# Kernel tuning notes

Hardware: AMD Instinct MI355X
Metric: run time of the kernel (lower is better)

The kernel has to match this reference:

```python
import jax, jax.numpy as jnp
import numpy as np

K = 2
ALPHA = 1.0
EPS = 1e-6


def _bce_logits(x, z):
    # binary_cross_entropy_with_logits, elementwise, numerically stable
    return jax.nn.softplus(x) - x * z


def _unfold(x, i):
    # F.unfold(x, kernel_size=2i+1, padding=i) for x: [B,1,H,W] -> [B, P, H*W]
    ks = 2 * i + 1
    p = jax.lax.conv_general_dilated_patches(
        x, (ks, ks), (1, 1), [(i, i), (i, i)])  # [B, ks*ks, H, W], zero-padded
    B = x.shape[0]
    return p.reshape(B, ks * ks, -1)


def setup_inputs() -> dict:
    key = jax.random.key(0)
    k1, k2 = jax.random.split(key)
    B, H, W = 8, 512, 512
    pred = jax.random.normal(k1, (B, 1, H, W), dtype=jnp.float32)
    target = jax.random.randint(k2, (B, 1, H, W), 0, 2).astype(jnp.float32)
    return {"pred": pred, "target": target}


def reference(pred, target):
    B, _, H, W = pred.shape
    N = H * W
    bce = _bce_logits(pred, target).reshape(B, 1, N)  # [B,1,N]
    total = jnp.zeros((B, N), dtype=pred.dtype)
    for i in range(1, K + 1):
        ks = 2 * i + 1
        P = ks * ks
        c = P // 2
        up = _unfold(pred, i)                      # [B,P,N]
        ut = _unfold(target, i)                    # [B,P,N]
        vm = _unfold(jnp.ones_like(target), i) == 0  # True where padding
        cp = up[:, c:c + 1, :]                     # center logits [B,1,N]
        ct = ut[:, c:c + 1, :]
        joint = cp * up
        lab = ct * ut
        mutual = _bce_logits(joint, lab)
        pairwise = jnp.exp(-jax.nn.sigmoid(cp) * jax.nn.sigmoid(up))
        loss = bce / (mutual + ALPHA * pairwise + EPS)
        loss = jnp.where(vm, jnp.asarray(1.0, loss.dtype), loss)
        total = total + (0.5 ** (i - 1)) * (loss.sum(axis=1) / P)
    return total.mean()
```

## Files before the change

### kernel.cpp

```cpp
#include <hip/hip_runtime.h>

#define TILE 16
#define HALO 2
#define LH (TILE + HALO)
#define LW (TILE + 2 * HALO)
#define HT 512
#define WD 512

typedef _Float16 h2 __attribute__((ext_vector_type(2)));

constexpr float W_IN  = 1.0f / 9.0f + 0.02f;
constexpr float W_OUT = 0.02f;
constexpr float INV_D_OOB = 0.590364f;


__device__ __forceinline__ h2 pk2(float a, float b) {
    return __builtin_bit_cast(h2, __builtin_amdgcn_cvt_pkrtz(a, b));
}
__device__ __forceinline__ h2 hsp(float x) {
    h2 r; r.x = (_Float16)x; r.y = (_Float16)x; return r;
}
__device__ __forceinline__ h2 mkh(float a, float b) {
    h2 r; r.x = (_Float16)a; r.y = (_Float16)b; return r;
}

struct FracH { h2 n, d; };

__device__ __forceinline__ FracH pair2h(float cax, h2 cay, h2 caz, h2 caw,
                                        const float4 cb1, const float4 cb2, h2 wv) {
    const float j1 = cax * cb1.x, j2 = cax * cb2.x;
    const h2 J = pk2(j1, j2);
    const h2 U = pk2(__expf(-fabsf(j1)), __expf(-fabsf(j2)));
    const h2 T = pk2(cb1.y, cb2.y);
    const h2 G = pk2(cb1.z, cb2.z);
    const h2 Wb = pk2(cb1.w, cb2.w);
    h2 L = __builtin_elementwise_fma(U, hsp(0.098765f), hsp(-0.370370f));
    L = __builtin_elementwise_fma(L, U, hsp(0.962963f));
    L = __builtin_elementwise_fma(L, U, hsp(0.004231f));
    const h2 LAB = T * cay;
    const h2 mx = __builtin_elementwise_max(J, hsp(0.f));
    h2 m = __builtin_elementwise_fma(-J, LAB, mx);
    m = m + L;
    const h2 GG = G * caz;
    h2 E = __builtin_elementwise_fma(GG, hsp(-0.101088f), hsp(0.454898f));
    E = __builtin_elementwise_fma(E, GG, hsp(-0.985612f));
    E = __builtin_elementwise_fma(E, GG, hsp(0.998280f));
    FracH r;
    r.d = m + E;
    r.n = (Wb + caw) * wv;
    return r;
}

__device__ __forceinline__ FracH mergeh(FracH a, FracH b) {
    FracH r;
    r.n = __builtin_elementwise_fma(a.n, b.d, a.d * b.n);
    r.d = a.d * b.d;
    return r;
}

__global__ __launch_bounds__(256) void scloss_main(
    const float* __restrict__ pred, const float* __restrict__ target,
    double* __restrict__ partial) {
    __shared__ float4 sh[LH * LW];

    const int b = blockIdx.x >> 10;
    const int tile = blockIdx.x & 1023;
    const int ty0 = (tile >> 5) << 4;
    const int tx0 = (tile & 31) << 4;

    const float* pbase = pred + ((size_t)b << 18);
    const float* tbase = target + ((size_t)b << 18);
    const int tid = threadIdx.x;

    #pragma unroll
    for (int i = 0; i < 2; ++i) {
        const int idx = tid + (i << 8);
        if (idx < LH * LW) {
            const int cy = idx / LW;
            const int cx = idx - cy * LW;
            const int gy = ty0 + cy;
            const int gx = tx0 + cx - HALO;
            float p = 0.f, t = 0.f, g = 0.f, bce = 0.f;
            if ((unsigned)gx < (unsigned)WD && gy < HT) {
                const int gi = (gy << 9) + gx;
                p = pbase[gi];
                t = tbase[gi];
                const float en = __expf(-fabsf(p));
                const float inv = __builtin_amdgcn_rcpf(1.f + en);
                g = (p >= 0.f) ? inv : en * inv;
                float L = fmaf(fmaf(fmaf(0.098765f, en, -0.370370f), en,
                                    0.962963f), en, 0.004231f);
                bce = fmaf(-p, t, fmaxf(p, 0.f)) + L;
            }
            sh[idx] = make_float4(p, t, g, bce);
        }
    }
    __syncthreads();

    const int px = tid & 15;
    const int py = tid >> 4;
    float acc = 0.f;

    const bool edge = (tx0 == 0) | (tx0 == WD - TILE) | (ty0 == 0) | (ty0 == HT - TILE);

    constexpr int pdy[12] = {0, 0, 1, 1, 1, 1, 1, 2, 2, 2, 2, 2};
    constexpr int pdx[12] = {1, 2, -2, -1, 0, 1, 2, -2, -1, 0, 1, 2};
    constexpr float pw12[12] = {W_IN, W_OUT, W_OUT, W_IN, W_IN, W_IN,
                                W_OUT, W_OUT, W_OUT, W_OUT, W_OUT, W_OUT};

    {
        const float4* base = &sh[py * LW + px + HALO];
        const float4 ca = base[0];

        const h2 cay = hsp(ca.y), caz = pk2(ca.z, ca.z), caw = pk2(ca.w, ca.w);

        const float j0 = ca.x * ca.x;
        const float u0 = __expf(-j0);
        const float L0 = fmaf(fmaf(fmaf(0.098765f, u0, -0.370370f), u0,
                                   0.962963f), u0, 0.004231f);
        const float m0 = fmaf(-j0, ca.y * ca.y, j0) + L0;
        const float gg0 = ca.z * ca.z;
        const float E0 = fmaf(fmaf(fmaf(-0.101088f, gg0, 0.454898f), gg0,
                                   -0.985612f), gg0, 0.998280f);
        const float d0 = m0 + E0;
        const float n0 = W_IN * ca.w;

        const FracH F1 = pair2h(ca.x, cay, caz, caw, base[1],          base[2],          mkh(W_IN,  W_OUT));
        const FracH F2 = pair2h(ca.x, cay, caz, caw, base[LW - 2],     base[LW - 1],     mkh(W_OUT, W_IN));
        const FracH F3 = pair2h(ca.x, cay, caz, caw, base[LW],         base[LW + 1],     mkh(W_IN,  W_IN));
        const FracH F4 = pair2h(ca.x, cay, caz, caw, base[LW + 2],     base[2 * LW - 2], mkh(W_OUT, W_OUT));
        const FracH F5 = pair2h(ca.x, cay, caz, caw, base[2 * LW - 1], base[2 * LW],     mkh(W_OUT, W_OUT));
        const FracH F6 = pair2h(ca.x, cay, caz, caw, base[2 * LW + 1], base[2 * LW + 2], mkh(W_OUT, W_OUT));

        const FracH A = mergeh(F1, F2);
        const FracH Bb = mergeh(F3, F4);
        const FracH C = mergeh(F5, F6);
        const FracH D2 = mergeh(A, Bb);
        const FracH G2 = mergeh(D2, C);

        const float nl = (float)G2.n.x, nh = (float)G2.n.y;
        const float dl = (float)G2.d.x, dh = (float)G2.d.y;
        const float Nt = fmaf(nl, dh, nh * dl), Dt = dl * dh;
        const float Nf = fmaf(n0, Dt, Nt * d0), Df = d0 * Dt;
        acc = fmaf(Nf, __builtin_amdgcn_rcpf(Df), acc);

        if (edge) {
            const int gy = ty0 + py, gx = tx0 + px;
            #pragma unroll
            for (int k = 0; k < 12; ++k) {
                if (gy + pdy[k] >= HT || gx + pdx[k] < 0 || gx + pdx[k] >= WD)
                    acc += pw12[k] * (1.f - ca.w * INV_D_OOB);
                if (gy - pdy[k] < 0 || gx - pdx[k] < 0 || gx - pdx[k] >= WD)
                    acc += pw12[k];
            }
        }
    }

    #pragma unroll
    for (int off = 32; off > 0; off >>= 1)
        acc += __shfl_down(acc, off, 64);
    __shared__ double wsum[4];
    if ((tid & 63) == 0) wsum[tid >> 6] = (double)acc;
    __syncthreads();
    if (tid == 0)
        partial[blockIdx.x] = wsum[0] + wsum[1] + wsum[2] + wsum[3];
}

__global__ __launch_bounds__(256) void scloss_reduce(
    const double* __restrict__ partial, int n, float* __restrict__ out,
    double inv_cnt) {
    __shared__ double sm[256];
    double s = 0.0;
    for (int i = threadIdx.x; i < n; i += 256) s += partial[i];
    sm[threadIdx.x] = s;
    __syncthreads();
    for (int off = 128; off > 0; off >>= 1) {
        if (threadIdx.x < off) sm[threadIdx.x] += sm[threadIdx.x + off];
        __syncthreads();
    }
    if (threadIdx.x == 0) out[0] = (float)(sm[0] * inv_cnt);
}

extern "C" void kernel_launch(void* const* d_in, const int* in_sizes, int n_in,
                              void* d_out, int out_size, void* d_ws, size_t ws_size,
                              hipStream_t stream) {
    const float* pred   = (const float*)d_in[0];
    const float* target = (const float*)d_in[1];
    float* out = (float*)d_out;

    const int B = in_sizes[0] / (HT * WD);
    const int nblocks = B * 1024;

    double* partial = (double*)d_ws;
    scloss_main<<<nblocks, 256, 0, stream>>>(pred, target, partial);
    scloss_reduce<<<1, 256, 0, stream>>>(partial, nblocks, out,
                                         1.0 / ((double)B * HT * WD));
}
```

Measured before the change: 92.04 us.

## Use persistent grid with double-buffered LDS and register prefetch of next tile

Replaces the one-block-per-tile launch with a fixed grid of 2048 persistent blocks that loop over tiles. Each block loads the next tile's inputs into registers while it computes the current tile from a double-buffered shared-memory array. Each wave writes its own partial sum directly, so the final block-level sync and shared reduction go away. This is meant to hide global load latency and cut block launch overhead. In exchange it uses twice the LDS and more registers, and each block gets only four tiles, so there is little pipeline depth.

```diff
diff --git a/kernel.cpp b/kernel.cpp
--- a/kernel.cpp
+++ b/kernel.cpp
@@ -4,15 +4,16 @@
 #define HALO 2
 #define LH (TILE + HALO)
 #define LW (TILE + 2 * HALO)
+#define NCELL (LH * LW)
 #define HT 512
 #define WD 512
+#define GRID 2048
 
 typedef _Float16 h2 __attribute__((ext_vector_type(2)));
 
 constexpr float W_IN  = 1.0f / 9.0f + 0.02f;
 constexpr float W_OUT = 0.02f;
 constexpr float INV_D_OOB = 0.590364f;
-
 
 __device__ __forceinline__ h2 pk2(float a, float b) {
     return __builtin_bit_cast(h2, __builtin_amdgcn_cvt_pkrtz(a, b));
@@ -58,58 +59,81 @@
     return r;
 }
 
+struct Pre { float p0, t0, p1, t1; bool v0, v1; };
+
+__device__ __forceinline__ Pre prefetch_tile(const float* __restrict__ pred,
+                                             const float* __restrict__ targ,
+                                             int t, int tid) {
+    const int b = t >> 10;
+    const int r = t & 1023;
+    const int ty0 = (r >> 5) << 4;
+    const int tx0 = (r & 31) << 4;
+    const float* pb = pred + ((size_t)b << 18);
+    const float* tb = targ + ((size_t)b << 18);
+    Pre o; o.p0 = 0.f; o.t0 = 0.f; o.p1 = 0.f; o.t1 = 0.f;
+    {
+        const int cy = tid / LW, cx = tid - cy * LW;
+        const int gy = ty0 + cy, gx = tx0 + cx - HALO;
+        o.v0 = ((unsigned)gx < (unsigned)WD) && (gy < HT);
+        if (o.v0) { const int gi = (gy << 9) + gx; o.p0 = pb[gi]; o.t0 = tb[gi]; }
+    }
+    {
+        const int idx = tid + 256;
+        const int cy = idx / LW, cx = idx - cy * LW;
+        const int gy = ty0 + cy, gx = tx0 + cx - HALO;
+        o.v1 = (idx < NCELL) && ((unsigned)gx < (unsigned)WD) && (gy < HT);
+        if (o.v1) { const int gi = (gy << 9) + gx; o.p1 = pb[gi]; o.t1 = tb[gi]; }
+    }
+    return o;
+}
+
+__device__ __forceinline__ float4 make_cell(float p, float t, bool valid) {
+    float4 c = make_float4(0.f, 0.f, 0.f, 0.f);
+    if (valid) {
+        const float en = __expf(-fabsf(p));
+        const float inv = __builtin_amdgcn_rcpf(1.f + en);
+        const float g = (p >= 0.f) ? inv : en * inv;
+        const float L = fmaf(fmaf(fmaf(0.098765f, en, -0.370370f), en,
+                                  0.962963f), en, 0.004231f);
+        const float bce = fmaf(-p, t, fmaxf(p, 0.f)) + L;
+        c = make_float4(p, t, g, bce);
+    }
+    return c;
+}
+
 __global__ __launch_bounds__(256) void scloss_main(
     const float* __restrict__ pred, const float* __restrict__ target,
-    double* __restrict__ partial) {
-    __shared__ float4 sh[LH * LW];
-
-    const int b = blockIdx.x >> 10;
-    const int tile = blockIdx.x & 1023;
-    const int ty0 = (tile >> 5) << 4;
-    const int tx0 = (tile & 31) << 4;
-
-    const float* pbase = pred + ((size_t)b << 18);
-    const float* tbase = target + ((size_t)b << 18);
+    double* __restrict__ partial, int total_tiles) {
+    __shared__ float4 sh[2][NCELL];
+
     const int tid = threadIdx.x;
-
-    #pragma unroll
-    for (int i = 0; i < 2; ++i) {
-        const int idx = tid + (i << 8);
-        if (idx < LH * LW) {
-            const int cy = idx / LW;
-            const int cx = idx - cy * LW;
-            const int gy = ty0 + cy;
-            const int gx = tx0 + cx - HALO;
-            float p = 0.f, t = 0.f, g = 0.f, bce = 0.f;
-            if ((unsigned)gx < (unsigned)WD && gy < HT) {
-                const int gi = (gy << 9) + gx;
-                p = pbase[gi];
-                t = tbase[gi];
-                const float en = __expf(-fabsf(p));
-                const float inv = __builtin_amdgcn_rcpf(1.f + en);
-                g = (p >= 0.f) ? inv : en * inv;
-                float L = fmaf(fmaf(fmaf(0.098765f, en, -0.370370f), en,
-                                    0.962963f), en, 0.004231f);
-                bce = fmaf(-p, t, fmaxf(p, 0.f)) + L;
-            }
-            sh[idx] = make_float4(p, t, g, bce);
-        }
-    }
-    __syncthreads();
-
-    const int px = tid & 15;
-    const int py = tid >> 4;
     float acc = 0.f;
-
-    const bool edge = (tx0 == 0) | (tx0 == WD - TILE) | (ty0 == 0) | (ty0 == HT - TILE);
 
     constexpr int pdy[12] = {0, 0, 1, 1, 1, 1, 1, 2, 2, 2, 2, 2};
     constexpr int pdx[12] = {1, 2, -2, -1, 0, 1, 2, -2, -1, 0, 1, 2};
     constexpr float pw12[12] = {W_IN, W_OUT, W_OUT, W_IN, W_IN, W_IN,
                                 W_OUT, W_OUT, W_OUT, W_OUT, W_OUT, W_OUT};
 
-    {
-        const float4* base = &sh[py * LW + px + HALO];
+    Pre cur = prefetch_tile(pred, target, blockIdx.x, tid);
+
+    int buf = 0;
+    for (int t = blockIdx.x; t < total_tiles; t += GRID, buf ^= 1) {
+        sh[buf][tid] = make_cell(cur.p0, cur.t0, cur.v0);
+        if (tid < NCELL - 256)
+            sh[buf][tid + 256] = make_cell(cur.p1, cur.t1, cur.v1);
+        __syncthreads();
+
+        const int tn = t + GRID;
+        if (tn < total_tiles)
+            cur = prefetch_tile(pred, target, tn, tid);
+
+        const int r = t & 1023;
+        const int ty0 = (r >> 5) << 4;
+        const int tx0 = (r & 31) << 4;
+        const int px = tid & 15;
+        const int py = tid >> 4;
+
+        const float4* base = &sh[buf][py * LW + px + HALO];
         const float4 ca = base[0];
 
         const h2 cay = hsp(ca.y), caz = pk2(ca.z, ca.z), caw = pk2(ca.w, ca.w);
@@ -132,9 +156,9 @@
         const FracH F5 = pair2h(ca.x, cay, caz, caw, base[2 * LW - 1], base[2 * LW],     mkh(W_OUT, W_OUT));
         const FracH F6 = pair2h(ca.x, cay, caz, caw, base[2 * LW + 1], base[2 * LW + 2], mkh(W_OUT, W_OUT));
 
-        const FracH A = mergeh(F1, F2);
+        const FracH A  = mergeh(F1, F2);
         const FracH Bb = mergeh(F3, F4);
-        const FracH C = mergeh(F5, F6);
+        const FracH C  = mergeh(F5, F6);
         const FracH D2 = mergeh(A, Bb);
         const FracH G2 = mergeh(D2, C);
 
@@ -144,6 +168,7 @@
         const float Nf = fmaf(n0, Dt, Nt * d0), Df = d0 * Dt;
         acc = fmaf(Nf, __builtin_amdgcn_rcpf(Df), acc);
 
+        const bool edge = (tx0 == 0) | (tx0 == WD - TILE) | (ty0 == 0) | (ty0 == HT - TILE);
         if (edge) {
             const int gy = ty0 + py, gx = tx0 + px;
             #pragma unroll
@@ -159,11 +184,8 @@
     #pragma unroll
     for (int off = 32; off > 0; off >>= 1)
         acc += __shfl_down(acc, off, 64);
-    __shared__ double wsum[4];
-    if ((tid & 63) == 0) wsum[tid >> 6] = (double)acc;
-    __syncthreads();
-    if (tid == 0)
-        partial[blockIdx.x] = wsum[0] + wsum[1] + wsum[2] + wsum[3];
+    if ((tid & 63) == 0)
+        partial[(blockIdx.x << 2) | (tid >> 6)] = (double)acc;
 }
 
 __global__ __launch_bounds__(256) void scloss_reduce(
@@ -189,10 +211,10 @@
     float* out = (float*)d_out;
 
     const int B = in_sizes[0] / (HT * WD);
-    const int nblocks = B * 1024;
+    const int total_tiles = B * 1024;
 
     double* partial = (double*)d_ws;
-    scloss_main<<<nblocks, 256, 0, stream>>>(pred, target, partial);
-    scloss_reduce<<<1, 256, 0, stream>>>(partial, nblocks, out,
+    scloss_main<<<GRID, 256, 0, stream>>>(pred, target, partial, total_tiles);
+    scloss_reduce<<<1, 256, 0, stream>>>(partial, GRID * 4, out,
                                          1.0 / ((double)B * HT * WD));
 }
```

Result: no change. 90.73 us (median of 2 runs) (-1.4%).
